# Kernel optimization log

Hardware: AMD Instinct MI355X
Metric: run time of the kernel (lower is better)

The kernel has to match this reference:

```python
import jax, jax.numpy as jnp
import numpy as np

NUM_USERS = 4000
NUM_LOCAS = 4000
D = 128            # embedding_dynamic_size
K = 64             # kg embedding dim
KG_ROWS = 5000
T = 2048           # number of events
IN_RNN = D + 1 + K # rnn input size (KG=True)
PRED_IN = NUM_USERS + NUM_LOCAS + 2 * D + K
PRED_OUT = NUM_LOCAS + D + K
EPS = 1e-12


def setup_inputs() -> dict:
    key = jax.random.key(0)
    ks = jax.random.split(key, 20)
    s = 0.05
    f32 = jnp.float32
    return {
        "embedding": jax.random.normal(ks[0], (NUM_USERS + NUM_LOCAS, D), f32),
        "events_int": jax.random.randint(ks[1], (T, 5), 0, 4000, dtype=jnp.int32),
        "delta_u": jax.random.uniform(ks[2], (T,), f32),
        "delta_l": jax.random.uniform(ks[3], (T,), f32),
        "kg": jax.random.normal(ks[4], (KG_ROWS, K), f32) * s,
        "w_ih_u": jax.random.normal(ks[5], (D, IN_RNN), f32) * s,
        "w_hh_u": jax.random.normal(ks[6], (D, D), f32) * s,
        "b_ih_u": jax.random.normal(ks[7], (D,), f32) * s,
        "b_hh_u": jax.random.normal(ks[8], (D,), f32) * s,
        "w_ih_l": jax.random.normal(ks[9], (D, IN_RNN), f32) * s,
        "w_hh_l": jax.random.normal(ks[10], (D, D), f32) * s,
        "b_ih_l": jax.random.normal(ks[11], (D,), f32) * s,
        "b_hh_l": jax.random.normal(ks[12], (D,), f32) * s,
        "proj_w": jax.random.normal(ks[13], (D, 1), f32) * s,
        "proj_b": jax.random.normal(ks[14], (D,), f32) * s,
        "pred_w": jax.random.normal(ks[15], (PRED_OUT, PRED_IN), f32) * s,
        "pred_b": jax.random.normal(ks[16], (PRED_OUT,), f32) * s,
    }


def _l2norm(x):
    # F.normalize(dim=-1) on a single row
    n = jnp.sqrt(jnp.sum(x * x))
    return x / jnp.maximum(n, EPS)


def reference(embedding, events_int, delta_u, delta_l, kg,
              w_ih_u, w_hh_u, b_ih_u, b_hh_u,
              w_ih_l, w_hh_l, b_ih_l, b_hh_l,
              proj_w, proj_b, pred_w, pred_b):
    # split prediction weight columns to match concat order:
    # [proj_user(D), emb_prev(D), kg_prev(K), static_loca(one-hot L), static_user(one-hot U)]
    W_proj_in = pred_w[:, :D]
    W_prev = pred_w[:, D:2 * D]
    W_kgp = pred_w[:, 2 * D:2 * D + K]
    W_sl = pred_w[:, 2 * D + K:2 * D + K + NUM_LOCAS]
    W_su = pred_w[:, 2 * D + K + NUM_LOCAS:]
    pw = proj_w[:, 0]

    def step(carry, ev):
        emb, loss = carry
        idx, du, dl = ev
        u, loca, prev, know_prev, know = idx[0], idx[1], idx[2], idx[3], idx[4]
        loca_g = loca + NUM_USERS
        prev_g = prev + NUM_USERS
        e_u = emb[u]        # [D]
        e_l = emb[loca_g]   # [D]
        e_p = emb[prev_g]   # [D]

        # projection: emb_user * (1 + Linear(1->D)(delta_u))
        proj = e_u * (1.0 + pw * du + proj_b)

        # prediction (one-hot static blocks -> column selects)
        pred = (W_proj_in @ proj + W_prev @ e_p + W_kgp @ kg[know_prev]
                + W_sl[:, prev] + W_su[:, u] + pred_b)
        one_hot_prev = jax.nn.one_hot(prev, NUM_LOCAS, dtype=emb.dtype)
        target = jax.lax.stop_gradient(
            jnp.concatenate([e_l, one_hot_prev, kg[know]]))
        loss = loss + jnp.mean((pred - target) ** 2)

        # RNNCell updates (tanh), inputs use pre-update embeddings
        inp_u = jnp.concatenate([e_l, kg[know], du[None]])
        new_u = _l2norm(jnp.tanh(w_ih_u @ inp_u + b_ih_u + w_hh_u @ e_u + b_hh_u))
        inp_l = jnp.concatenate([e_u, kg[know], dl[None]])
        new_l = _l2norm(jnp.tanh(w_ih_l @ inp_l + b_ih_l + w_hh_l @ e_l + b_hh_l))

        loss = loss + jnp.mean((new_u - jax.lax.stop_gradient(e_u)) ** 2)
        loss = loss + jnp.mean((new_l - jax.lax.stop_gradient(e_l)) ** 2)

        emb = emb.at[u].set(new_u).at[loca_g].set(new_l)
        return (emb, loss), None

    (emb_out, loss), _ = jax.lax.scan(
        step, (embedding, jnp.zeros((), embedding.dtype)),
        (events_int, delta_u, delta_l))
    return emb_out, loss
```

## Files before the change

kernel.cpp:

```cpp
#include <hip/hip_runtime.h>

#define T_STEPS 2048
#define NUSERS 4000
#define NLOCAS 4000
#define DD 128
#define KK 64
#define PRED_OUT 4192
#define PRED_IN 8256
#define OUT_EMB 1024000
#define TAIL_LV 8
#define WB_ROWS 4224

typedef __attribute__((ext_vector_type(8))) short short8v;
typedef __attribute__((ext_vector_type(4))) float f32x4;

#define WS_NEWU   0
#define WS_NEWL   262144
#define WS_KU     524288
#define WS_KL     786432
#define WS_ZB     1048576
#define WS_WB     1376256
#define WS_ELT    2052096
#define WS_DRIFT  2314240
#define WS_ROWP   2316288
#define WS_INT    2450432
#define WS_S      2464832
#define IO_PU     0
#define IO_PL     2048
#define IO_PP     4096
#define IO_LASTU  6144
#define IO_LASTL  8192
#define IO_ORDER  10240
#define IO_OFF    12288
#define IO_NLEV   14337

__device__ inline unsigned short f2bf(float f) {
    unsigned int x = __float_as_uint(f);
    unsigned int r = (x + 0x7FFFu + ((x >> 16) & 1u)) >> 16;
    return (unsigned short)r;
}

__global__ __launch_bounds__(256) void prep_kernel(const int* __restrict__ ev,
    const float* __restrict__ emb_in, const float* __restrict__ du,
    const float* __restrict__ dl, const float* __restrict__ kg,
    const float* __restrict__ wihu, const float* __restrict__ bihu,
    const float* __restrict__ bhhu, const float* __restrict__ wihl,
    const float* __restrict__ bihl, const float* __restrict__ bhhl,
    const float* __restrict__ predw,
    float* __restrict__ out, float* __restrict__ KU, float* __restrict__ KL,
    unsigned short* __restrict__ Wb, int* __restrict__ ibase) {
    __shared__ int su[T_STEPS];
    __shared__ int sl[T_STEPS];
    __shared__ float skg[4][KK];
    __shared__ int kn4[4];
    const int tid = threadIdx.x;

    if (blockIdx.x < 512) {
        const int lane = tid & 63;
        const int wid  = tid >> 6;
        for (int i = tid; i < T_STEPS; i += 256) { su[i] = ev[i*5]; sl[i] = ev[i*5+1]; }
        __syncthreads();

        const int t = blockIdx.x * 4 + wid;
        const int u = su[t], l = sl[t], p = ev[t*5 + 2];

        int pu = -1, pl = -1, pp = -1;
        {
            int round = 0;
            while (true) {
                const int q = t - 1 - lane - (round << 6);
                const int squ = (q >= 0) ? su[q] : -1;
                const int sql = (q >= 0) ? sl[q] : -1;
                if (pu < 0) {
                    unsigned long long b = __ballot(squ == u);
                    if (b) pu = t - 1 - (__ffsll(b) - 1) - (round << 6);
                }
                if (pl < 0) {
                    unsigned long long b = __ballot(sql == l);
                    if (b) pl = t - 1 - (__ffsll(b) - 1) - (round << 6);
                }
                if (pp < 0) {
                    unsigned long long b = __ballot(sql == p);
                    if (b) pp = t - 1 - (__ffsll(b) - 1) - (round << 6);
                }
                ++round;
                if ((pu >= 0 && pl >= 0 && pp >= 0) || (t - 1 - (round << 6) < 0)) break;
            }
        }
        int lastu = 1, lastl = 1;
        {
            int round = 0;
            while (true) {
                const int q = t + 1 + lane + (round << 6);
                const int squ = (q < T_STEPS) ? su[q] : -1;
                const int sql = (q < T_STEPS) ? sl[q] : -1;
                if (lastu && __ballot(squ == u)) lastu = 0;
                if (lastl && __ballot(sql == l)) lastl = 0;
                ++round;
                if ((!lastu && !lastl) || (t + 1 + (round << 6) >= T_STEPS)) break;
            }
        }
        if (lane == 0) {
            ibase[IO_PU + t] = pu;
            ibase[IO_PL + t] = pl;
            ibase[IO_PP + t] = pp;
            ibase[IO_LASTU + t] = lastu;
            ibase[IO_LASTL + t] = lastl;
        }
        return;
    }

    const int pb = blockIdx.x - 512;
    if (tid < 4) kn4[tid] = ev[(pb*4 + tid)*5 + 4];
    __syncthreads();
    skg[tid >> 6][tid & 63] = kg[kn4[tid >> 6]*KK + (tid & 63)];
    __syncthreads();
    #pragma unroll
    for (int p = 0; p < 2; ++p) {
        const int sub = p*2 + (tid >> 7);
        const int t = pb*4 + sub;
        const int r = tid & 127;
        const float* wu = wihu + r*193;
        const float* wl = wihl + r*193;
        const float dut = du[t], dlt = dl[t];
        float ku = bihu[r] + bhhu[r] + wu[192]*dut;
        float kl = bihl[r] + bhhl[r] + wl[192]*dlt;
        const float* sk = skg[sub];
        #pragma unroll
        for (int j = 0; j < KK; ++j) {
            float s = sk[j];
            ku += wu[128+j]*s;
            kl += wl[128+j]*s;
        }
        KU[t*DD + r] = ku;
        KL[t*DD + r] = kl;
    }

    const int gsz = 512 * 256;
    const int gid = pb * 256 + tid;
    for (int i = gid; i < OUT_EMB/4; i += gsz)
        ((float4*)out)[i] = ((const float4*)emb_in)[i];
    for (int i = gid; i < WB_ROWS*80; i += gsz) {
        int r = i / 80, kc = (i - r*80) * 4;
        unsigned short o0 = 0, o1 = 0, o2 = 0, o3 = 0;
        if (r < PRED_OUT) {
            const float4 v = *(const float4*)(predw + (size_t)r*PRED_IN + kc);
            o0 = f2bf(v.x); o1 = f2bf(v.y); o2 = f2bf(v.z); o3 = f2bf(v.w);
        }
        unsigned short* dst = Wb + (size_t)r*320 + kc;
        dst[0] = o0; dst[1] = o1; dst[2] = o2; dst[3] = o3;
    }
}

__global__ __launch_bounds__(1024) void levels_kernel(int* __restrict__ ibase) {
    __shared__ int lev[T_STEPS];
    __shared__ int spu[T_STEPS];
    __shared__ int spl[T_STEPS];
    __shared__ int cnt[T_STEPS + 1];
    __shared__ int changed;
    __shared__ int smax;
    const int tid = threadIdx.x;

    for (int i = tid; i < T_STEPS; i += 1024) {
        spu[i] = ibase[IO_PU + i];
        spl[i] = ibase[IO_PL + i];
        lev[i] = 0;
    }
    if (tid == 0) smax = 0;
    __syncthreads();

    while (true) {
        if (tid == 0) changed = 0;
        __syncthreads();
        for (int i = tid; i < T_STEPS; i += 1024) {
            int nl = 0, a = spu[i], b = spl[i];
            if (a >= 0) nl = lev[a] + 1;
            if (b >= 0) { int v = lev[b] + 1; if (v > nl) nl = v; }
            if (nl > lev[i]) { lev[i] = nl; changed = 1; }
        }
        __syncthreads();
        if (!changed) break;
        __syncthreads();
    }

    for (int i = tid; i <= T_STEPS; i += 1024) cnt[i] = 0;
    __syncthreads();
    for (int i = tid; i < T_STEPS; i += 1024) {
        atomicAdd(&cnt[lev[i]], 1);
        atomicMax(&smax, lev[i]);
    }
    __syncthreads();
    if (tid == 0) {
        int nlev = smax + 1;
        int acc = 0;
        for (int k = 0; k < nlev; ++k) {
            ibase[IO_OFF + k] = acc;
            int c = cnt[k]; cnt[k] = acc; acc += c;
        }
        ibase[IO_OFF + nlev] = acc;
        ibase[IO_NLEV] = nlev;
        for (int k = nlev + 1; k <= TAIL_LV; ++k) ibase[IO_OFF + k] = acc;
    }
    __syncthreads();
    for (int i = tid; i < T_STEPS; i += 1024) {
        int pos = atomicAdd(&cnt[lev[i]], 1);
        ibase[IO_ORDER + pos] = i;
    }
}

__global__ __launch_bounds__(512) void chain_sweep(int lv, const int* __restrict__ ev,
    const float* __restrict__ emb0,
    const float* __restrict__ wihu, const float* __restrict__ whhu,
    const float* __restrict__ whhl, const float* __restrict__ wihl,
    const float* __restrict__ KU, const float* __restrict__ KL,
    float* __restrict__ NEWU, float* __restrict__ NEWL, float* __restrict__ DRIFT,
    const int* __restrict__ ibase) {
    const int start = ibase[IO_OFF + lv];
    const int end   = ibase[IO_OFF + lv + 1];
    if ((int)blockIdx.x >= end - start) return;

    const int tid  = threadIdx.x;
    const int h    = tid >> 8;
    const int r    = tid & 255;
    const int lane = tid & 63;
    const int wid  = tid >> 6;

    float w[128];
    {
        const float* src;
        if (h == 0) src = (r < 128) ? (wihu + r*193) : (whhl + (r-128)*128);
        else        src = (r < 128) ? (whhu + r*128) : (wihl + (r-128)*193);
        #pragma unroll
        for (int j = 0; j < 32; ++j) {
            const float4 v = *(const float4*)(src + j*4);
            w[j*4+0] = v.x; w[j*4+1] = v.y; w[j*4+2] = v.z; w[j*4+3] = v.w;
        }
    }

    __shared__ float xs[256];
    __shared__ float partial[512];
    __shared__ float wsum[8];

    for (int s = start + blockIdx.x; s < end; s += gridDim.x) {
        const int t  = ibase[IO_ORDER + s];
        const int u  = ev[t*5];
        const int l  = ev[t*5 + 1];
        const int pu = ibase[IO_PU + t];
        const int pl = ibase[IO_PL + t];

        float kv = 0.f;
        if (tid < 128) {
            xs[tid] = (pl >= 0) ? NEWL[pl*DD + tid] : emb0[(size_t)(l + NUSERS)*DD + tid];
            kv = KU[t*DD + tid];
        } else if (tid < 256) {
            int d = tid - 128;
            xs[tid] = (pu >= 0) ? NEWU[pu*DD + d] : emb0[(size_t)u*DD + d];
            kv = KL[t*DD + d];
        }
        __syncthreads();

        float acc = 0.f;
        {
            const float* xp = xs + h*128;
            #pragma unroll
            for (int j = 0; j < 128; ++j) acc += w[j] * xp[j];
        }
        partial[tid] = acc;
        __syncthreads();

        float th = 0.f;
        if (tid < 256) {
            float pre = partial[tid] + partial[256 + tid] + kv;
            th = tanhf(pre);
            float ss = th * th;
            #pragma unroll
            for (int o = 32; o > 0; o >>= 1) ss += __shfl_xor(ss, o, 64);
            if (lane == 0) wsum[wid] = ss;
        }
        __syncthreads();

        if (tid < 256) {
            float S  = (tid < 128) ? (wsum[0] + wsum[1]) : (wsum[2] + wsum[3]);
            float sf = 1.f / fmaxf(sqrtf(S), 1e-12f);
            float v2 = th * sf;
            float old = (tid < 128) ? xs[128 + tid] : xs[tid - 128];
            if (tid < 128) NEWU[t*DD + tid]       = v2;
            else           NEWL[t*DD + (tid-128)] = v2;
            float dd = v2 - old;
            float s2 = dd * dd;
            #pragma unroll
            for (int o = 32; o > 0; o >>= 1) s2 += __shfl_xor(s2, o, 64);
            if (lane == 0) wsum[4 + wid] = s2;
        }
        __syncthreads();
        if (tid == 0)
            DRIFT[t] = (wsum[4] + wsum[5] + wsum[6] + wsum[7]) * (1.f / 128.f);
    }
}

__global__ __launch_bounds__(512) void chain_tail(const int* __restrict__ ev,
    const float* __restrict__ emb0,
    const float* __restrict__ wihu, const float* __restrict__ whhu,
    const float* __restrict__ whhl, const float* __restrict__ wihl,
    const float* __restrict__ KU, const float* __restrict__ KL,
    float* __restrict__ NEWU, float* __restrict__ NEWL, float* __restrict__ DRIFT,
    const int* __restrict__ ibase) {
    const int nlev = ibase[IO_NLEV];
    if (nlev <= TAIL_LV) return;
    const int start = ibase[IO_OFF + TAIL_LV];
    const int end   = ibase[IO_OFF + nlev];

    const int tid  = threadIdx.x;
    const int h    = tid >> 8;
    const int r    = tid & 255;
    const int lane = tid & 63;
    const int wid  = tid >> 6;

    float w[128];
    {
        const float* src;
        if (h == 0) src = (r < 128) ? (wihu + r*193) : (whhl + (r-128)*128);
        else        src = (r < 128) ? (whhu + r*128) : (wihl + (r-128)*193);
        #pragma unroll
        for (int j = 0; j < 32; ++j) {
            const float4 v = *(const float4*)(src + j*4);
            w[j*4+0] = v.x; w[j*4+1] = v.y; w[j*4+2] = v.z; w[j*4+3] = v.w;
        }
    }

    __shared__ float xs[256];
    __shared__ float partial[512];
    __shared__ float wsum[8];

    for (int s = start; s < end; ++s) {
        const int t  = ibase[IO_ORDER + s];
        const int u  = ev[t*5];
        const int l  = ev[t*5 + 1];
        const int pu = ibase[IO_PU + t];
        const int pl = ibase[IO_PL + t];

        float kv = 0.f;
        if (tid < 128) {
            xs[tid] = (pl >= 0) ? NEWL[pl*DD + tid] : emb0[(size_t)(l + NUSERS)*DD + tid];
            kv = KU[t*DD + tid];
        } else if (tid < 256) {
            int d = tid - 128;
            xs[tid] = (pu >= 0) ? NEWU[pu*DD + d] : emb0[(size_t)u*DD + d];
            kv = KL[t*DD + d];
        }
        __syncthreads();

        float acc = 0.f;
        {
            const float* xp = xs + h*128;
            #pragma unroll
            for (int j = 0; j < 128; ++j) acc += w[j] * xp[j];
        }
        partial[tid] = acc;
        __syncthreads();

        float th = 0.f;
        if (tid < 256) {
            float pre = partial[tid] + partial[256 + tid] + kv;
            th = tanhf(pre);
            float ss = th * th;
            #pragma unroll
            for (int o = 32; o > 0; o >>= 1) ss += __shfl_xor(ss, o, 64);
            if (lane == 0) wsum[wid] = ss;
        }
        __syncthreads();

        if (tid < 256) {
            float S  = (tid < 128) ? (wsum[0] + wsum[1]) : (wsum[2] + wsum[3]);
            float sf = 1.f / fmaxf(sqrtf(S), 1e-12f);
            float v2 = th * sf;
            float old = (tid < 128) ? xs[128 + tid] : xs[tid - 128];
            if (tid < 128) NEWU[t*DD + tid]       = v2;
            else           NEWL[t*DD + (tid-128)] = v2;
            float dd = v2 - old;
            float s2 = dd * dd;
            #pragma unroll
            for (int o = 32; o > 0; o >>= 1) s2 += __shfl_xor(s2, o, 64);
            if (lane == 0) wsum[4 + wid] = s2;
        }
        __syncthreads();
        if (tid == 0)
            DRIFT[t] = (wsum[4] + wsum[5] + wsum[6] + wsum[7]) * (1.f / 128.f);
    }
}

__global__ __launch_bounds__(256) void build_z(const int* __restrict__ ev,
    const float* __restrict__ emb0, const float* __restrict__ du,
    const float* __restrict__ pw, const float* __restrict__ projb,
    const float* __restrict__ kg,
    const float* __restrict__ NEWU, const float* __restrict__ NEWL,
    unsigned short* __restrict__ Zb, float* __restrict__ ELT,
    float* __restrict__ out, const int* __restrict__ ibase) {
    const int gsz = gridDim.x * blockDim.x;
    const int gid = blockIdx.x * blockDim.x + threadIdx.x;

    for (int i = gid; i < T_STEPS*320; i += gsz) {
        int t = i / 320, j = i - t*320;
        float zv;
        if (j < 128) {
            int pu = ibase[IO_PU + t];
            int uu = ev[t*5];
            float eu = (pu >= 0) ? NEWU[pu*DD + j] : emb0[(size_t)uu*DD + j];
            zv = eu * (1.f + pw[j]*du[t] + projb[j]);
        } else if (j < 256) {
            int jj = j - 128;
            int pp = ibase[IO_PP + t];
            int pv = ev[t*5 + 2];
            zv = (pp >= 0) ? NEWL[pp*DD + jj] : emb0[(size_t)(pv + NUSERS)*DD + jj];
        } else {
            int kp = ev[t*5 + 3];
            zv = kg[kp*KK + (j - 256)];
        }
        Zb[i] = f2bf(zv);
    }
    for (int i = gid; i < DD*T_STEPS; i += gsz) {
        int d = i >> 11, t = i & 2047;
        int pl = ibase[IO_PL + t];
        int l  = ev[t*5 + 1];
        ELT[i] = (pl >= 0) ? NEWL[pl*DD + d] : emb0[(size_t)(l + NUSERS)*DD + d];
    }
    for (int i = gid; i < T_STEPS*DD; i += gsz) {
        int t = i >> 7, d = i & 127;
        if (ibase[IO_LASTU + t]) out[(size_t)ev[t*5]*DD + d]            = NEWU[i];
        if (ibase[IO_LASTL + t]) out[(size_t)(ev[t*5+1]+NUSERS)*DD + d] = NEWL[i];
    }
}

__global__ __launch_bounds__(256) void pred_dense_mfma(
    const unsigned short* __restrict__ Wb, const unsigned short* __restrict__ Zb,
    float* __restrict__ S, int NT, int t0) {
    const int tid = threadIdx.x;
    const int l   = tid & 63;
    const int w   = tid >> 6;
    const int wr  = w >> 1, wc = w & 1;
    const int lr  = l & 15;
    const int kg8 = (l >> 4) * 8;
    const int r0  = blockIdx.y * 128 + wr * 64;
    const int tt0 = blockIdx.x * 128 + wc * 64;

    f32x4 acc[4][4];
    #pragma unroll
    for (int m = 0; m < 4; ++m)
        #pragma unroll
        for (int n = 0; n < 4; ++n) acc[m][n] = (f32x4){0.f, 0.f, 0.f, 0.f};

    for (int k0 = 0; k0 < 320; k0 += 32) {
        short8v a[4], b[4];
        #pragma unroll
        for (int m = 0; m < 4; ++m)
            a[m] = *(const short8v*)(Wb + (size_t)(r0 + m*16 + lr)*320 + k0 + kg8);
        #pragma unroll
        for (int n = 0; n < 4; ++n)
            b[n] = *(const short8v*)(Zb + (size_t)(t0 + tt0 + n*16 + lr)*320 + k0 + kg8);
        #pragma unroll
        for (int m = 0; m < 4; ++m)
            #pragma unroll
            for (int n = 0; n < 4; ++n)
                acc[m][n] = __builtin_amdgcn_mfma_f32_16x16x32_bf16(a[m], b[n], acc[m][n], 0, 0, 0);
    }

    const int orow = (l >> 4) * 4;
    #pragma unroll
    for (int m = 0; m < 4; ++m) {
        #pragma unroll
        for (int i = 0; i < 4; ++i) {
            int r = r0 + m*16 + orow + i;
            if (r < PRED_OUT) {
                float* dst = S + (size_t)r*NT + tt0 + lr;
                #pragma unroll
                for (int n = 0; n < 4; ++n) dst[n*16] = acc[m][n][i];
            }
        }
    }
}

__global__ __launch_bounds__(256) void pred_scatter(const int* __restrict__ ev,
    const float* __restrict__ predw, const float* __restrict__ predb,
    const float* __restrict__ kg, const float* __restrict__ S,
    const float* __restrict__ ELT, float* __restrict__ rowp,
    int NT, int t0, int chunk) {
    __shared__ float srow[NLOCAS + NUSERS];
    __shared__ float red[4];
    const int tid = threadIdx.x;
    const int lane = tid & 63, wid = tid >> 6;
    const int r = blockIdx.x;
    const float* base = predw + (size_t)r*PRED_IN + 320;
    #pragma unroll
    for (int i = 0; i < 8; ++i) {
        int idx = (tid + i*256) * 4;
        if (idx < NLOCAS + NUSERS) {
            float4 v = *(const float4*)(base + idx);
            *(float4*)(srow + idx) = v;
        }
    }
    __syncthreads();
    const float bias = predb[r];
    const int mode = (r < DD) ? 0 : (r < DD + NLOCAS ? 1 : 2);
    float lsum = 0.f;
    for (int tb = tid*4; tb < NT; tb += 1024) {
        const float4 sv = *(const float4*)(S + (size_t)r*NT + tb);
        const float sa[4] = {sv.x, sv.y, sv.z, sv.w};
        #pragma unroll
        for (int q = 0; q < 4; ++q) {
            int t = t0 + tb + q;
            int pv = ev[t*5 + 2];
            int uu = ev[t*5 + 0];
            float v = sa[q] + bias + srow[pv] + srow[NLOCAS + uu];
            float tv;
            if (mode == 0)      tv = ELT[r*T_STEPS + t];
            else if (mode == 1) tv = (pv == r - DD) ? 1.f : 0.f;
            else                tv = kg[ev[t*5+4]*KK + (r - DD - NLOCAS)];
            float d = v - tv;
            lsum += d*d;
        }
    }
    #pragma unroll
    for (int o = 32; o > 0; o >>= 1) lsum += __shfl_xor(lsum, o, 64);
    if (lane == 0) red[wid] = lsum;
    __syncthreads();
    if (tid == 0) rowp[chunk*PRED_OUT + r] = red[0] + red[1] + red[2] + red[3];
}

__global__ __launch_bounds__(256) void final_reduce(const float* __restrict__ rowp,
                                                    const float* __restrict__ drift,
                                                    float* __restrict__ out, int nchunk) {
    int tid = threadIdx.x;
    float s = 0.f;
    for (int i = tid; i < nchunk*PRED_OUT; i += 256) s += rowp[i];
    s *= (1.0f / PRED_OUT);
    for (int i = tid; i < T_STEPS; i += 256) s += drift[i];
    #pragma unroll
    for (int o = 32; o > 0; o >>= 1) s += __shfl_xor(s, o, 64);
    __shared__ float red[4];
    if ((tid & 63) == 0) red[tid >> 6] = s;
    __syncthreads();
    if (tid == 0) out[OUT_EMB] = red[0] + red[1] + red[2] + red[3];
}

extern "C" void kernel_launch(void* const* d_in, const int* in_sizes, int n_in,
                              void* d_out, int out_size, void* d_ws, size_t ws_size,
                              hipStream_t stream) {
    const float* emb_in = (const float*)d_in[0];
    const int*   ev     = (const int*)  d_in[1];
    const float* du     = (const float*)d_in[2];
    const float* dl     = (const float*)d_in[3];
    const float* kg     = (const float*)d_in[4];
    const float* wihu   = (const float*)d_in[5];
    const float* whhu   = (const float*)d_in[6];
    const float* bihu   = (const float*)d_in[7];
    const float* bhhu   = (const float*)d_in[8];
    const float* wihl   = (const float*)d_in[9];
    const float* whhl   = (const float*)d_in[10];
    const float* bihl   = (const float*)d_in[11];
    const float* bhhl   = (const float*)d_in[12];
    const float* projw  = (const float*)d_in[13];
    const float* projb  = (const float*)d_in[14];
    const float* predw  = (const float*)d_in[15];
    const float* predb  = (const float*)d_in[16];

    float* out = (float*)d_out;
    float* ws  = (float*)d_ws;
    float* NEWU  = ws + WS_NEWU;
    float* NEWL  = ws + WS_NEWL;
    float* KU    = ws + WS_KU;
    float* KL    = ws + WS_KL;
    unsigned short* Zb = (unsigned short*)(ws + WS_ZB);
    unsigned short* Wb = (unsigned short*)(ws + WS_WB);
    float* ELT   = ws + WS_ELT;
    float* DRIFT = ws + WS_DRIFT;
    float* ROWP  = ws + WS_ROWP;
    float* S     = ws + WS_S;
    int*   ibase = (int*)(ws + WS_INT);

    long avail = (long)(ws_size / 4) - WS_S;
    int NT = 2048;
    while (NT > 128 && (long)PRED_OUT * NT > avail) NT >>= 1;
    int nchunk = T_STEPS / NT;

    prep_kernel<<<1024, 256, 0, stream>>>(ev, emb_in, du, dl, kg,
                                          wihu, bihu, bhhu, wihl, bihl, bhhl,
                                          predw, out, KU, KL, Wb, ibase);
    levels_kernel<<<1, 1024, 0, stream>>>(ibase);
    for (int lv = 0; lv < TAIL_LV; ++lv)
        chain_sweep<<<256, 512, 0, stream>>>(lv, ev, emb_in, wihu, whhu, whhl, wihl,
                                             KU, KL, NEWU, NEWL, DRIFT, ibase);
    chain_tail<<<1, 512, 0, stream>>>(ev, emb_in, wihu, whhu, whhl, wihl,
                                      KU, KL, NEWU, NEWL, DRIFT, ibase);
    build_z<<<1024, 256, 0, stream>>>(ev, emb_in, du, projw, projb, kg,
                                      NEWU, NEWL, Zb, ELT, out, ibase);
    for (int c = 0; c < nchunk; ++c) {
        int t0 = c * NT;
        pred_dense_mfma<<<dim3(NT/128, 33), 256, 0, stream>>>(Wb, Zb, S, NT, t0);
        pred_scatter<<<PRED_OUT, 256, 0, stream>>>(ev, predw, predb, kg, S, ELT,
                                                   ROWP, NT, t0, c);
    }
    final_reduce<<<1, 256, 0, stream>>>(ROWP, DRIFT, out, nchunk);
}
```

Measured before the change: 204.3 us.

## Store prediction scores as bf16 and prefetch packed event indices in scatter

The dense MFMA kernel now writes its score matrix as bf16 instead of fp32, halving the size of the large intermediate written and re-read by the scatter kernel. build_z packs each event's prev-location, user and know indices into one int4 array. pred_scatter issues its score, index and ELT loads before the shared-memory row fill and barrier, and each thread handles 8 timesteps. The number of parallel chain-sweep levels also drops from 8 to 6, moving more work to the single-block tail. Rounding the scores to bf16 adds error to the loss, and the sweep/tail split change shifts serial work onto the tail.

```diff
diff --git a/kernel.cpp b/kernel.cpp
--- a/kernel.cpp
+++ b/kernel.cpp
@@ -8,10 +8,11 @@
 #define PRED_OUT 4192
 #define PRED_IN 8256
 #define OUT_EMB 1024000
-#define TAIL_LV 8
+#define TAIL_LV 6
 #define WB_ROWS 4224
 
 typedef __attribute__((ext_vector_type(8))) short short8v;
+typedef __attribute__((ext_vector_type(8))) unsigned short ushort8v;
 typedef __attribute__((ext_vector_type(4))) float f32x4;
 
 #define WS_NEWU   0
@@ -24,7 +25,8 @@
 #define WS_DRIFT  2314240
 #define WS_ROWP   2316288
 #define WS_INT    2450432
-#define WS_S      2464832
+#define WS_PVU    2464832
+#define WS_S      2473024
 #define IO_PU     0
 #define IO_PL     2048
 #define IO_PP     4096
@@ -38,6 +40,9 @@
     unsigned int x = __float_as_uint(f);
     unsigned int r = (x + 0x7FFFu + ((x >> 16) & 1u)) >> 16;
     return (unsigned short)r;
+}
+__device__ inline float bf2f(unsigned short u) {
+    return __uint_as_float(((unsigned int)u) << 16);
 }
 
 __global__ __launch_bounds__(256) void prep_kernel(const int* __restrict__ ev,
@@ -395,9 +400,13 @@
     const float* __restrict__ kg,
     const float* __restrict__ NEWU, const float* __restrict__ NEWL,
     unsigned short* __restrict__ Zb, float* __restrict__ ELT,
+    int4* __restrict__ PVU,
     float* __restrict__ out, const int* __restrict__ ibase) {
     const int gsz = gridDim.x * blockDim.x;
     const int gid = blockIdx.x * blockDim.x + threadIdx.x;
+
+    for (int i = gid; i < T_STEPS; i += gsz)
+        PVU[i] = make_int4(ev[i*5 + 2], ev[i*5 + 0], ev[i*5 + 4], 0);
 
     for (int i = gid; i < T_STEPS*320; i += gsz) {
         int t = i / 320, j = i - t*320;
@@ -433,7 +442,7 @@
 
 __global__ __launch_bounds__(256) void pred_dense_mfma(
     const unsigned short* __restrict__ Wb, const unsigned short* __restrict__ Zb,
-    float* __restrict__ S, int NT, int t0) {
+    unsigned short* __restrict__ S, int NT, int t0) {
     const int tid = threadIdx.x;
     const int l   = tid & 63;
     const int w   = tid >> 6;
@@ -471,17 +480,17 @@
         for (int i = 0; i < 4; ++i) {
             int r = r0 + m*16 + orow + i;
             if (r < PRED_OUT) {
-                float* dst = S + (size_t)r*NT + tt0 + lr;
+                unsigned short* dst = S + (size_t)r*NT + tt0 + lr;
                 #pragma unroll
-                for (int n = 0; n < 4; ++n) dst[n*16] = acc[m][n][i];
+                for (int n = 0; n < 4; ++n) dst[n*16] = f2bf(acc[m][n][i]);
             }
         }
     }
 }
 
-__global__ __launch_bounds__(256) void pred_scatter(const int* __restrict__ ev,
+__global__ __launch_bounds__(256) void pred_scatter(const int4* __restrict__ PVU,
     const float* __restrict__ predw, const float* __restrict__ predb,
-    const float* __restrict__ kg, const float* __restrict__ S,
+    const float* __restrict__ kg, const unsigned short* __restrict__ S,
     const float* __restrict__ ELT, float* __restrict__ rowp,
     int NT, int t0, int chunk) {
     __shared__ float srow[NLOCAS + NUSERS];
@@ -489,6 +498,22 @@
     const int tid = threadIdx.x;
     const int lane = tid & 63, wid = tid >> 6;
     const int r = blockIdx.x;
+    const int mode = (r < DD) ? 0 : (r < DD + NLOCAS ? 1 : 2);
+    const bool active = tid < (NT >> 3);
+
+    ushort8v sv = (ushort8v)0;
+    int4 pq[8];
+    float4 e0 = make_float4(0,0,0,0), e1 = make_float4(0,0,0,0);
+    if (active) {
+        sv = *(const ushort8v*)(S + (size_t)r*NT + tid*8);
+        #pragma unroll
+        for (int q = 0; q < 8; ++q) pq[q] = PVU[t0 + tid*8 + q];
+        if (mode == 0) {
+            e0 = *(const float4*)(ELT + r*T_STEPS + t0 + tid*8);
+            e1 = *(const float4*)(ELT + r*T_STEPS + t0 + tid*8 + 4);
+        }
+    }
+
     const float* base = predw + (size_t)r*PRED_IN + 320;
     #pragma unroll
     for (int i = 0; i < 8; ++i) {
@@ -499,22 +524,20 @@
         }
     }
     __syncthreads();
+
     const float bias = predb[r];
-    const int mode = (r < DD) ? 0 : (r < DD + NLOCAS ? 1 : 2);
+    const int kcol = r - DD - NLOCAS;
     float lsum = 0.f;
-    for (int tb = tid*4; tb < NT; tb += 1024) {
-        const float4 sv = *(const float4*)(S + (size_t)r*NT + tb);
-        const float sa[4] = {sv.x, sv.y, sv.z, sv.w};
-        #pragma unroll
-        for (int q = 0; q < 4; ++q) {
-            int t = t0 + tb + q;
-            int pv = ev[t*5 + 2];
-            int uu = ev[t*5 + 0];
-            float v = sa[q] + bias + srow[pv] + srow[NLOCAS + uu];
+    if (active) {
+        const float ee[8] = {e0.x, e0.y, e0.z, e0.w, e1.x, e1.y, e1.z, e1.w};
+        #pragma unroll
+        for (int q = 0; q < 8; ++q) {
+            const int pv = pq[q].x, uu = pq[q].y, kn = pq[q].z;
+            float v = bf2f(sv[q]) + bias + srow[pv] + srow[NLOCAS + uu];
             float tv;
-            if (mode == 0)      tv = ELT[r*T_STEPS + t];
+            if (mode == 0)      tv = ee[q];
             else if (mode == 1) tv = (pv == r - DD) ? 1.f : 0.f;
-            else                tv = kg[ev[t*5+4]*KK + (r - DD - NLOCAS)];
+            else                tv = kg[kn*KK + kcol];
             float d = v - tv;
             lsum += d*d;
         }
@@ -574,12 +597,13 @@
     float* ELT   = ws + WS_ELT;
     float* DRIFT = ws + WS_DRIFT;
     float* ROWP  = ws + WS_ROWP;
-    float* S     = ws + WS_S;
+    int4*  PVU   = (int4*)(ws + WS_PVU);
+    unsigned short* S = (unsigned short*)(ws + WS_S);
     int*   ibase = (int*)(ws + WS_INT);
 
-    long avail = (long)(ws_size / 4) - WS_S;
+    long cap = ((long)ws_size - (long)WS_S*4) / 2;
     int NT = 2048;
-    while (NT > 128 && (long)PRED_OUT * NT > avail) NT >>= 1;
+    while (NT > 128 && (long)PRED_OUT * NT > cap) NT >>= 1;
     int nchunk = T_STEPS / NT;
 
     prep_kernel<<<1024, 256, 0, stream>>>(ev, emb_in, du, dl, kg,
@@ -592,11 +616,11 @@
     chain_tail<<<1, 512, 0, stream>>>(ev, emb_in, wihu, whhu, whhl, wihl,
                                       KU, KL, NEWU, NEWL, DRIFT, ibase);
     build_z<<<1024, 256, 0, stream>>>(ev, emb_in, du, projw, projb, kg,
-                                      NEWU, NEWL, Zb, ELT, out, ibase);
+                                      NEWU, NEWL, Zb, ELT, PVU, out, ibase);
     for (int c = 0; c < nchunk; ++c) {
         int t0 = c * NT;
         pred_dense_mfma<<<dim3(NT/128, 33), 256, 0, stream>>>(Wb, Zb, S, NT, t0);
-        pred_scatter<<<PRED_OUT, 256, 0, stream>>>(ev, predw, predb, kg, S, ELT,
+        pred_scatter<<<PRED_OUT, 256, 0, stream>>>(PVU, predw, predb, kg, S, ELT,
                                                    ROWP, NT, t0, c);
     }
     final_reduce<<<1, 256, 0, stream>>>(ROWP, DRIFT, out, nchunk);
```

Result: faster. 190.3 us (-6.9%).
